# Kernel tuning notes

Hardware: AMD Instinct MI355X
Metric: run time of the kernel (lower is better)

## Reference

```python
import jax, jax.numpy as jnp
import numpy as np

N, E = 50000, 800000
IN_F, OUT_F = 256, 128


def setup_inputs() -> dict:
    key = jax.random.key(0)
    ks = jax.random.split(key, 12)
    s = 1.0 / np.sqrt(OUT_F)
    si = 1.0 / np.sqrt(IN_F)
    return {
        "h": jax.random.normal(ks[0], (N, IN_F), jnp.float32),
        "degrees": jax.random.randint(ks[1], (E, 6), 0, 5).astype(jnp.float32),
        "norm": jax.random.uniform(ks[2], (N, 1), jnp.float32, 0.05, 1.0),
        "src": jax.random.randint(ks[3], (E,), 0, N, jnp.int32),
        "dst": jax.random.randint(ks[4], (E,), 0, N, jnp.int32),
        "W_self": jax.random.normal(ks[5], (IN_F, OUT_F), jnp.float32) * si,
        "b_self": jax.random.normal(ks[6], (OUT_F,), jnp.float32) * si,
        "W_node": jax.random.normal(ks[7], (IN_F, 6 * OUT_F), jnp.float32) * si,
        "b_node": jax.random.normal(ks[8], (6 * OUT_F,), jnp.float32) * si,
        "W_edge": jax.random.normal(ks[9], (6, OUT_F), jnp.float32) * 0.4,
        "bias": jax.random.normal(ks[10], (1, OUT_F), jnp.float32) * 2 * s - s,
    }


def reference(h, degrees, norm, src, dst, W_self, b_self, W_node, b_node, W_edge, bias):
    n = h.shape[0]
    out = W_self.shape[1]
    # node-level linears
    h_node_msg = (h @ W_node + b_node).reshape(n, 6, out)  # [N,6,out]
    h_node_self = h @ W_self + b_self                       # [N,out]
    # edge-level linear (no bias)
    msg = degrees @ W_edge                                  # [E,out]
    mask = (degrees > 0).astype(h.dtype)                    # [E,6]
    # masked sum over the 6 degree-conditioned slices (gather per slice to
    # avoid materializing an [E,6,out] tensor)
    for i in range(6):
        msg = msg + h_node_msg[src, i] * mask[:, i:i + 1]
    msg = msg * norm[src]                                   # src-side norm
    accum = jax.ops.segment_sum(msg, dst, num_segments=n) * norm  # dst-side norm
    return jax.nn.relu(accum + h_node_self + bias)
```

## Files before the change

kernel.cpp:

```cpp
#include <hip/hip_runtime.h>
#include <stdint.h>

#define IN_F 256
#define OUT_F 128
#define NCOLS 1024
#define PROW 1280
#define BM 64
#define BN 128
#define BK 32

using bf16x8 = __attribute__((ext_vector_type(8))) __bf16;
using f32x4  = __attribute__((ext_vector_type(4))) float;
using f32x2  = __attribute__((ext_vector_type(2))) float;

static __device__ __forceinline__ unsigned short f2bf(float f) {
    unsigned u = __float_as_uint(f);
    u = u + 0x7fffu + ((u >> 16) & 1u);
    return (unsigned short)(u >> 16);
}
static __device__ __forceinline__ float bf_lo(unsigned u) { return __uint_as_float(u << 16); }
static __device__ __forceinline__ float bf_hi(unsigned u) { return __uint_as_float(u & 0xffff0000u); }

static __device__ __forceinline__ void async_load16(const void* g, void* l) {
    __builtin_amdgcn_global_load_lds(
        (__attribute__((address_space(1))) void*)g,
        (__attribute__((address_space(3))) void*)l,
        16, 0, 0);
}

__global__ void k_conv_h(const float* __restrict__ h, unsigned short* __restrict__ hb, int total8) {
    int i = blockIdx.x * blockDim.x + threadIdx.x;
    if (i >= total8) return;
    const float4* src = ((const float4*)h) + (size_t)i * 2;
    float4 a = src[0], b = src[1];
    union { unsigned short us[8]; uint4 v; } u;
    u.us[0] = f2bf(a.x); u.us[1] = f2bf(a.y); u.us[2] = f2bf(a.z); u.us[3] = f2bf(a.w);
    u.us[4] = f2bf(b.x); u.us[5] = f2bf(b.y); u.us[6] = f2bf(b.z); u.us[7] = f2bf(b.w);
    ((uint4*)hb)[i] = u.v;
}

__global__ void k_conv_w(const float* __restrict__ Wn, const float* __restrict__ Ws,
                         const float* __restrict__ bn, const float* __restrict__ bs,
                         unsigned short* __restrict__ Wt, float* __restrict__ bvec, int total) {
    int i = blockIdx.x * blockDim.x + threadIdx.x;
    if (i >= total) return;
    int k = i >> 10, c = i & 1023;
    float v;
    if (c < 768) {
        v = Wn[(size_t)k * 768 + c];
    } else if (c < 896) {
        int j = c - 768; v = 0.f;
#pragma unroll
        for (int s = 0; s < 6; ++s) v += Wn[(size_t)k * 768 + s * 128 + j];
    } else {
        v = Ws[(size_t)k * 128 + (c - 896)];
    }
    Wt[(size_t)c * IN_F + k] = f2bf(v);

    if (i < NCOLS) {
        float b;
        if (i < 768) b = bn[i];
        else if (i < 896) {
            int j = i - 768; b = 0.f;
#pragma unroll
            for (int s = 0; s < 6; ++s) b += bn[s * 128 + j];
        } else b = bs[i - 896];
        bvec[i] = b;
    }
}

__global__ void __launch_bounds__(256) k_gemm(
    const unsigned short* __restrict__ hb,
    const unsigned short* __restrict__ Wt,
    const float* __restrict__ bvec,
    const float* __restrict__ norm,
    char* __restrict__ PG, int N, int rowsPerXcd)
{
    __shared__ char lds[(BM + BN) * BK * 2];
    char* Ab = lds;
    char* Bb = lds + BM * BK * 2;

    const int f  = blockIdx.x;
    const int xc = f & 7;
    const int j  = f >> 3;
    const int rs = xc * rowsPerXcd + (j >> 3);
    const int ct = j & 7;
    const int r0 = rs * BM;
    if (r0 >= N) return;
    const int c0 = ct * BN;

    const int tid = threadIdx.x;
    const int wid = tid >> 6, lane = tid & 63;
    const int lrow = lane & 15, s = lane >> 4;
    const int wr = wid >> 1, wc = wid & 1;

    const int arow = tid >> 2;
    const int achunk = (tid & 3) ^ ((arow >> 1) & 3);
    int agrow = r0 + arow; if (agrow >= N) agrow = N - 1;
    const unsigned short* aseg = hb + (size_t)agrow * IN_F + achunk * 8;

    const int bcol0 = tid >> 2;
    const int bchunk0 = (tid & 3) ^ ((bcol0 >> 1) & 3);
    const unsigned short* bseg0 = Wt + (size_t)(c0 + bcol0) * IN_F + bchunk0 * 8;
    const int idx1 = tid + 256;
    const int bcol1 = idx1 >> 2;
    const int bchunk1 = (idx1 & 3) ^ ((bcol1 >> 1) & 3);
    const unsigned short* bseg1 = Wt + (size_t)(c0 + bcol1) * IN_F + bchunk1 * 8;

    int a_off[2], b_off[4];
#pragma unroll
    for (int m = 0; m < 2; ++m) {
        int rl = wr * 32 + m * 16 + lrow;
        a_off[m] = rl * 64 + ((s ^ ((rl >> 1) & 3)) << 4);
    }
#pragma unroll
    for (int n = 0; n < 4; ++n) {
        int cl = wc * 64 + n * 16 + lrow;
        b_off[n] = cl * 64 + ((s ^ ((cl >> 1) & 3)) << 4);
    }

    float nrmv[2][4];
#pragma unroll
    for (int m = 0; m < 2; ++m)
#pragma unroll
        for (int r = 0; r < 4; ++r) {
            int rg = r0 + wr * 32 + m * 16 + s * 4 + r;
            nrmv[m][r] = norm[rg < N ? rg : N - 1];
        }

    f32x4 acc[2][4] = {};

    for (int kk = 0; kk < IN_F / BK; ++kk) {
        async_load16(aseg + kk * BK, Ab + tid * 16);
        async_load16(bseg0 + kk * BK, Bb + tid * 16);
        async_load16(bseg1 + kk * BK, Bb + (tid + 256) * 16);
        __syncthreads();

        bf16x8 af[2], bfv[4];
#pragma unroll
        for (int m = 0; m < 2; ++m) af[m] = *(const bf16x8*)(Ab + a_off[m]);
#pragma unroll
        for (int n = 0; n < 4; ++n) bfv[n] = *(const bf16x8*)(Bb + b_off[n]);
#pragma unroll
        for (int m = 0; m < 2; ++m)
#pragma unroll
            for (int n = 0; n < 4; ++n)
                acc[m][n] = __builtin_amdgcn_mfma_f32_16x16x32_bf16(af[m], bfv[n], acc[m][n], 0, 0, 0);
        __syncthreads();
    }

    float bvn[4];
#pragma unroll
    for (int n = 0; n < 4; ++n) bvn[n] = bvec[c0 + wc * 64 + n * 16 + lrow];

    if (ct < 6) {
#pragma unroll
        for (int m = 0; m < 2; ++m) {
#pragma unroll
            for (int r = 0; r < 4; ++r) {
                const int rg = r0 + wr * 32 + m * 16 + s * 4 + r;
                const float sc = nrmv[m][r];
                float v0 = (acc[m][0][r] + bvn[0]) * sc;
                float v1 = (acc[m][1][r] + bvn[1]) * sc;
                float v2 = (acc[m][2][r] + bvn[2]) * sc;
                float v3 = (acc[m][3][r] + bvn[3]) * sc;
                int d = __builtin_amdgcn_cvt_pk_fp8_f32(v0, v1, 0, false);
                d = __builtin_amdgcn_cvt_pk_fp8_f32(v2, v3, d, true);
                if (rg < N)
                    *(int*)(PG + (size_t)rg * PROW + ct * 128 + (wc * 16 + lrow) * 4) = d;
            }
        }
    } else {
        const bool doN = (ct == 6);
        const int boff = doN ? 768 : 1024;
#pragma unroll
        for (int m = 0; m < 2; ++m) {
#pragma unroll
            for (int r = 0; r < 4; ++r) {
                const int rg = r0 + wr * 32 + m * 16 + s * 4 + r;
                const float sc = doN ? nrmv[m][r] : 1.f;
                float v0 = (acc[m][0][r] + bvn[0]) * sc;
                float v1 = (acc[m][1][r] + bvn[1]) * sc;
                float v2 = (acc[m][2][r] + bvn[2]) * sc;
                float v3 = (acc[m][3][r] + bvn[3]) * sc;
                uint2 dd;
                dd.x = (unsigned)f2bf(v0) | ((unsigned)f2bf(v1) << 16);
                dd.y = (unsigned)f2bf(v2) | ((unsigned)f2bf(v3) << 16);
                if (rg < N)
                    *(uint2*)(PG + (size_t)rg * PROW + boff + (wc * 32 + 2 * lrow) * 4) = dd;
            }
        }
    }
}

__global__ void k_hist(const int* __restrict__ dst, int* __restrict__ counts, int E) {
    int e = blockIdx.x * blockDim.x + threadIdx.x;
    if (e < E) atomicAdd(&counts[dst[e]], 1);
}

__global__ void __launch_bounds__(256) k_scan_a(const int* __restrict__ counts,
                                                int* __restrict__ offs,
                                                int* __restrict__ bsum, int N) {
    __shared__ int sm[256];
    int tid = threadIdx.x;
    int i = blockIdx.x * 256 + tid;
    int v = (i < N) ? counts[i] : 0;
    sm[tid] = v;
    __syncthreads();
#pragma unroll
    for (int st = 1; st < 256; st <<= 1) {
        int t = (tid >= st) ? sm[tid - st] : 0;
        __syncthreads();
        sm[tid] += t;
        __syncthreads();
    }
    if (i < N) offs[i] = sm[tid] - v;
    if (tid == 255) bsum[blockIdx.x] = sm[255];
}

__global__ void __launch_bounds__(256) k_scan_b(int* __restrict__ bsum, int NB) {
    __shared__ int sm[256];
    int tid = threadIdx.x;
    int v = (tid < NB) ? bsum[tid] : 0;
    sm[tid] = v;
    __syncthreads();
#pragma unroll
    for (int st = 1; st < 256; st <<= 1) {
        int t = (tid >= st) ? sm[tid - st] : 0;
        __syncthreads();
        sm[tid] += t;
        __syncthreads();
    }
    if (tid < NB) bsum[tid] = sm[tid] - v;
}

__global__ void k_scan_c(int* __restrict__ offs, const int* __restrict__ bsum,
                         int* __restrict__ cursor, int N) {
    int i = blockIdx.x * 256 + threadIdx.x;
    if (i >= N) return;
    int o = offs[i] + bsum[blockIdx.x];
    offs[i] = o;
    cursor[i] = o;
}

__global__ void k_scatter(const int* __restrict__ src, const int* __restrict__ dst,
                          const float* __restrict__ degrees,
                          int* __restrict__ cursor, uint2* __restrict__ pedge, int E) {
    int e = blockIdx.x * blockDim.x + threadIdx.x;
    if (e >= E) return;
    int d = dst[e];
    int slot = atomicAdd(&cursor[d], 1);
    unsigned pk = 0;
#pragma unroll
    for (int i = 0; i < 6; ++i) {
        float df = degrees[(size_t)e * 6 + i];
        pk |= ((unsigned)df) << (4 * i);
    }
    pedge[slot] = make_uint2((unsigned)src[e], pk);
}

__global__ void __launch_bounds__(256) k_aggregate(
    const char* __restrict__ PG,
    const int* __restrict__ row_start, const int* __restrict__ counts,
    const uint2* __restrict__ pedge,
    const float* __restrict__ norm, const float* __restrict__ W_edge,
    const float* __restrict__ bias, float* __restrict__ out, int N)
{
    __shared__ unsigned ELS[4][64];
    __shared__ unsigned ELF[4][192];
    const int wid = threadIdx.x >> 6;
    const int n = blockIdx.x * 4 + wid;
    if (n >= N) return;
    const int lane = threadIdx.x & 63;
    unsigned* els = ELS[wid];
    unsigned* elf = ELF[wid];

    const int cA = (lane >> 5) * 64 + (lane & 1) * 32 + ((lane >> 1) & 15);
    const int cB = cA + 16;

    float wA[6], wB[6];
#pragma unroll
    for (int i = 0; i < 6; ++i) {
        wA[i] = W_edge[i * OUT_F + cA];
        wB[i] = W_edge[i * OUT_F + cB];
    }

    const int beg = row_start[n];
    const int end = beg + counts[n];

    float Swd[6] = {0.f, 0.f, 0.f, 0.f, 0.f, 0.f};
    float g0 = 0.f, g1 = 0.f;

    for (int p0 = beg; p0 < end; p0 += 64) {
        const int t = p0 + lane;
        uint2 pe = (t < end) ? pedge[t] : make_uint2(0u, 0u);
        const unsigned dp = pe.y;
        const float nr = (dp != 0u) ? norm[pe.x] : 0.f;

        unsigned zm = 0;
#pragma unroll
        for (int i = 0; i < 6; ++i) {
            int d = (dp >> (4 * i)) & 15;
            if (d == 0) zm |= (1u << i);
            Swd[i] += nr * (float)d;
        }
        const int z = __popc(zm);
        int ns, nf;
        if (dp == 0u)      { ns = 0; nf = 0; }
        else if (z <= 2)   { ns = 1; nf = z; }
        else               { ns = 0; nf = 6 - z; }

        int x = (ns << 16) | nf;
#pragma unroll
        for (int st = 1; st < 64; st <<= 1) {
            int v = __shfl_up(x, st);
            if (lane >= st) x += v;
        }
        const int tot = __shfl(x, 63);
        x -= (ns << 16) | nf;
        const int exS = x >> 16, exF = x & 0xffff;
        const int totS = tot >> 16, totF = tot & 0xffff;

        if (dp != 0u) {
            const unsigned base = pe.x * (unsigned)PROW;
            if (z <= 2) {
                els[exS] = base + 768u;
                int wp = exF;
#pragma unroll
                for (int i = 0; i < 6; ++i)
                    if ((zm >> i) & 1u) elf[wp++] = (base + i * 128u) | 0x80000000u;
            } else {
                int wp = exF;
#pragma unroll
                for (int i = 0; i < 6; ++i)
                    if (!((zm >> i) & 1u)) elf[wp++] = base + i * 128u;
            }
        }
        asm volatile("s_waitcnt lgkmcnt(0)" ::: "memory");

        int j = 0;
        for (; j + 4 <= totS; j += 4) {
            unsigned a0 = els[j], a1 = els[j + 1], a2 = els[j + 2], a3 = els[j + 3];
            unsigned u0 = *(const unsigned*)(PG + a0 + lane * 4);
            unsigned u1 = *(const unsigned*)(PG + a1 + lane * 4);
            unsigned u2 = *(const unsigned*)(PG + a2 + lane * 4);
            unsigned u3 = *(const unsigned*)(PG + a3 + lane * 4);
            g0 += bf_lo(u0); g1 += bf_hi(u0);
            g0 += bf_lo(u1); g1 += bf_hi(u1);
            g0 += bf_lo(u2); g1 += bf_hi(u2);
            g0 += bf_lo(u3); g1 += bf_hi(u3);
        }
        for (; j < totS; ++j) {
            unsigned u0 = *(const unsigned*)(PG + els[j] + lane * 4);
            g0 += bf_lo(u0); g1 += bf_hi(u0);
        }

        j = 0;
        for (; j + 4 <= totF; j += 4) {
            unsigned e0 = elf[j], e1 = elf[j + 1], e2 = elf[j + 2], e3 = elf[j + 3];
            unsigned short q0 = *(const unsigned short*)(PG + (e0 & 0x7fffffffu) + lane * 2);
            unsigned short q1 = *(const unsigned short*)(PG + (e1 & 0x7fffffffu) + lane * 2);
            unsigned short q2 = *(const unsigned short*)(PG + (e2 & 0x7fffffffu) + lane * 2);
            unsigned short q3 = *(const unsigned short*)(PG + (e3 & 0x7fffffffu) + lane * 2);
            f32x2 f0 = __builtin_amdgcn_cvt_pk_f32_fp8((int)q0, false);
            f32x2 f1 = __builtin_amdgcn_cvt_pk_f32_fp8((int)q1, false);
            f32x2 f2 = __builtin_amdgcn_cvt_pk_f32_fp8((int)q2, false);
            f32x2 f3 = __builtin_amdgcn_cvt_pk_f32_fp8((int)q3, false);
            float s0 = __uint_as_float(0x3f800000u | (e0 & 0x80000000u));
            float s1 = __uint_as_float(0x3f800000u | (e1 & 0x80000000u));
            float s2 = __uint_as_float(0x3f800000u | (e2 & 0x80000000u));
            float s3 = __uint_as_float(0x3f800000u | (e3 & 0x80000000u));
            g0 += s0 * f0.x; g1 += s0 * f0.y;
            g0 += s1 * f1.x; g1 += s1 * f1.y;
            g0 += s2 * f2.x; g1 += s2 * f2.y;
            g0 += s3 * f3.x; g1 += s3 * f3.y;
        }
        for (; j < totF; ++j) {
            unsigned e0 = elf[j];
            unsigned short q0 = *(const unsigned short*)(PG + (e0 & 0x7fffffffu) + lane * 2);
            f32x2 f0 = __builtin_amdgcn_cvt_pk_f32_fp8((int)q0, false);
            float s0 = __uint_as_float(0x3f800000u | (e0 & 0x80000000u));
            g0 += s0 * f0.x; g1 += s0 * f0.y;
        }
    }

    float b0 = 0.f, b1 = 0.f;
#pragma unroll
    for (int i = 0; i < 6; ++i) {
        float v = Swd[i];
#pragma unroll
        for (int st = 1; st < 64; st <<= 1) v += __shfl_xor(v, st);
        b0 += v * wA[i];
        b1 += v * wB[i];
    }

    const unsigned us = *(const unsigned*)(PG + (size_t)n * PROW + 1024 + lane * 4);
    const float nd = norm[n];
    float o0 = fmaxf((g0 + b0) * nd + bf_lo(us) + bias[cA], 0.f);
    float o1 = fmaxf((g1 + b1) * nd + bf_hi(us) + bias[cB], 0.f);
    out[(size_t)n * OUT_F + cA] = o0;
    out[(size_t)n * OUT_F + cB] = o1;
}

extern "C" void kernel_launch(void* const* d_in, const int* in_sizes, int n_in,
                              void* d_out, int out_size, void* d_ws, size_t ws_size,
                              hipStream_t stream)
{
    const float* h       = (const float*)d_in[0];
    const float* degrees = (const float*)d_in[1];
    const float* norm    = (const float*)d_in[2];
    const int*   src     = (const int*)d_in[3];
    const int*   dst     = (const int*)d_in[4];
    const float* W_self  = (const float*)d_in[5];
    const float* b_self  = (const float*)d_in[6];
    const float* W_node  = (const float*)d_in[7];
    const float* b_node  = (const float*)d_in[8];
    const float* W_edge  = (const float*)d_in[9];
    const float* bias    = (const float*)d_in[10];
    float* out = (float*)d_out;

    const int N = in_sizes[2];
    const int E = in_sizes[3];
    const int NB = (N + 255) / 256;

    char* ws = (char*)d_ws;
    size_t off = 0;
    auto alloc = [&](size_t sz) { size_t o = off; off = (off + sz + 255) & ~(size_t)255; return o; };
    char*           PG     = (char*)(ws + alloc((size_t)N * PROW));
    unsigned short* hb     = (unsigned short*)(ws + alloc((size_t)N * IN_F * 2));
    unsigned short* Wt     = (unsigned short*)(ws + alloc((size_t)NCOLS * IN_F * 2));
    float*          bvec   = (float*)(ws + alloc(NCOLS * 4));
    int*            counts = (int*)(ws + alloc((size_t)N * 4));
    int*            offs   = (int*)(ws + alloc((size_t)N * 4));
    int*            cursor = (int*)(ws + alloc((size_t)N * 4));
    int*            bsum   = (int*)(ws + alloc((size_t)NB * 4));
    uint2*          pedge  = (uint2*)(ws + alloc((size_t)E * 8));

    hipMemsetAsync(counts, 0, (size_t)N * 4, stream);

    int t8 = N * (IN_F / 8);
    k_conv_h<<<(t8 + 255) / 256, 256, 0, stream>>>(h, hb, t8);

    int tw = IN_F * NCOLS;
    k_conv_w<<<(tw + 255) / 256, 256, 0, stream>>>(W_node, W_self, b_node, b_self, Wt, bvec, tw);

    const int R  = (N + BM - 1) / BM;
    const int RP = (R + 7) / 8;
    k_gemm<<<RP * 8 * 8, 256, 0, stream>>>(hb, Wt, bvec, norm, PG, N, RP);

    k_hist<<<(E + 255) / 256, 256, 0, stream>>>(dst, counts, E);
    k_scan_a<<<NB, 256, 0, stream>>>(counts, offs, bsum, N);
    k_scan_b<<<1, 256, 0, stream>>>(bsum, NB);
    k_scan_c<<<NB, 256, 0, stream>>>(offs, bsum, cursor, N);
    k_scatter<<<(E + 255) / 256, 256, 0, stream>>>(src, dst, degrees, cursor, pedge, E);

    k_aggregate<<<(N + 3) / 4, 256, 0, stream>>>(PG, offs, counts, pedge, norm, W_edge, bias, out, N);
}
```

Baseline: 248.8 us.

## Interleave per-node message slices into 1KB rows, drop summed-slice GEMM columns

The projected-feature buffer is re-laid out so each node row is 1024 bytes, with each lane's six fp8 slice values plus its bf16 self term packed contiguously in 16 bytes. The GEMM no longer computes the extra 'sum of all six slices' column tile, so the grid drops from eight to seven column tiles. The aggregation kernel replaces its per-wavefront prefix-scan compaction of nonzero slices with one 16-byte load per edge and mask-multiplied FMAs. This trades the sparse-gather bookkeeping for always loading all six slices per edge, and it uses scattered 2-byte stores in the GEMM epilogue.

```diff
diff --git a/kernel.cpp b/kernel.cpp
--- a/kernel.cpp
+++ b/kernel.cpp
@@ -3,8 +3,8 @@
 
 #define IN_F 256
 #define OUT_F 128
-#define NCOLS 1024
-#define PROW 1280
+#define NCOLSG 896
+#define PROW 1024
 #define BM 64
 #define BN 128
 #define BK 32
@@ -44,29 +44,10 @@
                          unsigned short* __restrict__ Wt, float* __restrict__ bvec, int total) {
     int i = blockIdx.x * blockDim.x + threadIdx.x;
     if (i >= total) return;
-    int k = i >> 10, c = i & 1023;
-    float v;
-    if (c < 768) {
-        v = Wn[(size_t)k * 768 + c];
-    } else if (c < 896) {
-        int j = c - 768; v = 0.f;
-#pragma unroll
-        for (int s = 0; s < 6; ++s) v += Wn[(size_t)k * 768 + s * 128 + j];
-    } else {
-        v = Ws[(size_t)k * 128 + (c - 896)];
-    }
+    int k = i / NCOLSG, c = i - k * NCOLSG;
+    float v = (c < 768) ? Wn[(size_t)k * 768 + c] : Ws[(size_t)k * 128 + (c - 768)];
     Wt[(size_t)c * IN_F + k] = f2bf(v);
-
-    if (i < NCOLS) {
-        float b;
-        if (i < 768) b = bn[i];
-        else if (i < 896) {
-            int j = i - 768; b = 0.f;
-#pragma unroll
-            for (int s = 0; s < 6; ++s) b += bn[s * 128 + j];
-        } else b = bs[i - 896];
-        bvec[i] = b;
-    }
+    if (i < NCOLSG) bvec[i] = (i < 768) ? bn[i] : bs[i - 768];
 }
 
 __global__ void __launch_bounds__(256) k_gemm(
@@ -83,8 +64,8 @@
     const int f  = blockIdx.x;
     const int xc = f & 7;
     const int j  = f >> 3;
-    const int rs = xc * rowsPerXcd + (j >> 3);
-    const int ct = j & 7;
+    const int rs = xc * rowsPerXcd + j / 7;
+    const int ct = j % 7;
     const int r0 = rs * BM;
     if (r0 >= N) return;
     const int c0 = ct * BN;
@@ -152,6 +133,7 @@
     float bvn[4];
 #pragma unroll
     for (int n = 0; n < 4; ++n) bvn[n] = bvec[c0 + wc * 64 + n * 16 + lrow];
+    const int L0 = wc * 32 + 2 * lrow;
 
     if (ct < 6) {
 #pragma unroll
@@ -159,35 +141,33 @@
 #pragma unroll
             for (int r = 0; r < 4; ++r) {
                 const int rg = r0 + wr * 32 + m * 16 + s * 4 + r;
+                if (rg >= N) continue;
                 const float sc = nrmv[m][r];
                 float v0 = (acc[m][0][r] + bvn[0]) * sc;
                 float v1 = (acc[m][1][r] + bvn[1]) * sc;
                 float v2 = (acc[m][2][r] + bvn[2]) * sc;
                 float v3 = (acc[m][3][r] + bvn[3]) * sc;
-                int d = __builtin_amdgcn_cvt_pk_fp8_f32(v0, v1, 0, false);
-                d = __builtin_amdgcn_cvt_pk_fp8_f32(v2, v3, d, true);
-                if (rg < N)
-                    *(int*)(PG + (size_t)rg * PROW + ct * 128 + (wc * 16 + lrow) * 4) = d;
+                int p01 = __builtin_amdgcn_cvt_pk_fp8_f32(v0, v1, 0, false);
+                int p23 = __builtin_amdgcn_cvt_pk_fp8_f32(v2, v3, 0, false);
+                char* base = PG + ((size_t)rg << 10) + L0 * 16 + ct * 2;
+                *(unsigned short*)(base)      = (unsigned short)p01;
+                *(unsigned short*)(base + 16) = (unsigned short)p23;
             }
         }
     } else {
-        const bool doN = (ct == 6);
-        const int boff = doN ? 768 : 1024;
 #pragma unroll
         for (int m = 0; m < 2; ++m) {
 #pragma unroll
             for (int r = 0; r < 4; ++r) {
                 const int rg = r0 + wr * 32 + m * 16 + s * 4 + r;
-                const float sc = doN ? nrmv[m][r] : 1.f;
-                float v0 = (acc[m][0][r] + bvn[0]) * sc;
-                float v1 = (acc[m][1][r] + bvn[1]) * sc;
-                float v2 = (acc[m][2][r] + bvn[2]) * sc;
-                float v3 = (acc[m][3][r] + bvn[3]) * sc;
-                uint2 dd;
-                dd.x = (unsigned)f2bf(v0) | ((unsigned)f2bf(v1) << 16);
-                dd.y = (unsigned)f2bf(v2) | ((unsigned)f2bf(v3) << 16);
-                if (rg < N)
-                    *(uint2*)(PG + (size_t)rg * PROW + boff + (wc * 32 + 2 * lrow) * 4) = dd;
+                if (rg >= N) continue;
+                float v0 = acc[m][0][r] + bvn[0];
+                float v1 = acc[m][1][r] + bvn[1];
+                float v2 = acc[m][2][r] + bvn[2];
+                float v3 = acc[m][3][r] + bvn[3];
+                char* base = PG + ((size_t)rg << 10) + L0 * 16 + 12;
+                *(unsigned*)(base)      = (unsigned)f2bf(v0) | ((unsigned)f2bf(v1) << 16);
+                *(unsigned*)(base + 16) = (unsigned)f2bf(v2) | ((unsigned)f2bf(v3) << 16);
             }
         }
     }
@@ -259,6 +239,22 @@
     pedge[slot] = make_uint2((unsigned)src[e], pk);
 }
 
+static __device__ __forceinline__ void edge_proc(uint4 v, unsigned dp, float& g0, float& g1) {
+    f32x2 f; float m;
+    m = (dp & 0x00000Fu) ? 1.f : 0.f; f = __builtin_amdgcn_cvt_pk_f32_fp8((int)v.x, false);
+    g0 = fmaf(m, f.x, g0); g1 = fmaf(m, f.y, g1);
+    m = (dp & 0x0000F0u) ? 1.f : 0.f; f = __builtin_amdgcn_cvt_pk_f32_fp8((int)v.x, true);
+    g0 = fmaf(m, f.x, g0); g1 = fmaf(m, f.y, g1);
+    m = (dp & 0x000F00u) ? 1.f : 0.f; f = __builtin_amdgcn_cvt_pk_f32_fp8((int)v.y, false);
+    g0 = fmaf(m, f.x, g0); g1 = fmaf(m, f.y, g1);
+    m = (dp & 0x00F000u) ? 1.f : 0.f; f = __builtin_amdgcn_cvt_pk_f32_fp8((int)v.y, true);
+    g0 = fmaf(m, f.x, g0); g1 = fmaf(m, f.y, g1);
+    m = (dp & 0x0F0000u) ? 1.f : 0.f; f = __builtin_amdgcn_cvt_pk_f32_fp8((int)v.z, false);
+    g0 = fmaf(m, f.x, g0); g1 = fmaf(m, f.y, g1);
+    m = (dp & 0xF00000u) ? 1.f : 0.f; f = __builtin_amdgcn_cvt_pk_f32_fp8((int)v.z, true);
+    g0 = fmaf(m, f.x, g0); g1 = fmaf(m, f.y, g1);
+}
+
 __global__ void __launch_bounds__(256) k_aggregate(
     const char* __restrict__ PG,
     const int* __restrict__ row_start, const int* __restrict__ counts,
@@ -266,17 +262,15 @@
     const float* __restrict__ norm, const float* __restrict__ W_edge,
     const float* __restrict__ bias, float* __restrict__ out, int N)
 {
-    __shared__ unsigned ELS[4][64];
-    __shared__ unsigned ELF[4][192];
+    __shared__ uint2 EB[4][64];
     const int wid = threadIdx.x >> 6;
     const int n = blockIdx.x * 4 + wid;
     if (n >= N) return;
     const int lane = threadIdx.x & 63;
-    unsigned* els = ELS[wid];
-    unsigned* elf = ELF[wid];
 
     const int cA = (lane >> 5) * 64 + (lane & 1) * 32 + ((lane >> 1) & 15);
     const int cB = cA + 16;
+    const int laneB = lane * 16;
 
     float wA[6], wB[6];
 #pragma unroll
@@ -296,91 +290,36 @@
         uint2 pe = (t < end) ? pedge[t] : make_uint2(0u, 0u);
         const unsigned dp = pe.y;
         const float nr = (dp != 0u) ? norm[pe.x] : 0.f;
-
-        unsigned zm = 0;
 #pragma unroll
         for (int i = 0; i < 6; ++i) {
             int d = (dp >> (4 * i)) & 15;
-            if (d == 0) zm |= (1u << i);
             Swd[i] += nr * (float)d;
         }
-        const int z = __popc(zm);
-        int ns, nf;
-        if (dp == 0u)      { ns = 0; nf = 0; }
-        else if (z <= 2)   { ns = 1; nf = z; }
-        else               { ns = 0; nf = 6 - z; }
-
-        int x = (ns << 16) | nf;
-#pragma unroll
-        for (int st = 1; st < 64; st <<= 1) {
-            int v = __shfl_up(x, st);
-            if (lane >= st) x += v;
-        }
-        const int tot = __shfl(x, 63);
-        x -= (ns << 16) | nf;
-        const int exS = x >> 16, exF = x & 0xffff;
-        const int totS = tot >> 16, totF = tot & 0xffff;
-
-        if (dp != 0u) {
-            const unsigned base = pe.x * (unsigned)PROW;
-            if (z <= 2) {
-                els[exS] = base + 768u;
-                int wp = exF;
-#pragma unroll
-                for (int i = 0; i < 6; ++i)
-                    if ((zm >> i) & 1u) elf[wp++] = (base + i * 128u) | 0x80000000u;
-            } else {
-                int wp = exF;
-#pragma unroll
-                for (int i = 0; i < 6; ++i)
-                    if (!((zm >> i) & 1u)) elf[wp++] = base + i * 128u;
-            }
-        }
+        EB[wid][lane] = pe;
         asm volatile("s_waitcnt lgkmcnt(0)" ::: "memory");
 
-        int j = 0;
-        for (; j + 4 <= totS; j += 4) {
-            unsigned a0 = els[j], a1 = els[j + 1], a2 = els[j + 2], a3 = els[j + 3];
-            unsigned u0 = *(const unsigned*)(PG + a0 + lane * 4);
-            unsigned u1 = *(const unsigned*)(PG + a1 + lane * 4);
-            unsigned u2 = *(const unsigned*)(PG + a2 + lane * 4);
-            unsigned u3 = *(const unsigned*)(PG + a3 + lane * 4);
-            g0 += bf_lo(u0); g1 += bf_hi(u0);
-            g0 += bf_lo(u1); g1 += bf_hi(u1);
-            g0 += bf_lo(u2); g1 += bf_hi(u2);
-            g0 += bf_lo(u3); g1 += bf_hi(u3);
-        }
-        for (; j < totS; ++j) {
-            unsigned u0 = *(const unsigned*)(PG + els[j] + lane * 4);
-            g0 += bf_lo(u0); g1 += bf_hi(u0);
-        }
-
-        j = 0;
-        for (; j + 4 <= totF; j += 4) {
-            unsigned e0 = elf[j], e1 = elf[j + 1], e2 = elf[j + 2], e3 = elf[j + 3];
-            unsigned short q0 = *(const unsigned short*)(PG + (e0 & 0x7fffffffu) + lane * 2);
-            unsigned short q1 = *(const unsigned short*)(PG + (e1 & 0x7fffffffu) + lane * 2);
-            unsigned short q2 = *(const unsigned short*)(PG + (e2 & 0x7fffffffu) + lane * 2);
-            unsigned short q3 = *(const unsigned short*)(PG + (e3 & 0x7fffffffu) + lane * 2);
-            f32x2 f0 = __builtin_amdgcn_cvt_pk_f32_fp8((int)q0, false);
-            f32x2 f1 = __builtin_amdgcn_cvt_pk_f32_fp8((int)q1, false);
-            f32x2 f2 = __builtin_amdgcn_cvt_pk_f32_fp8((int)q2, false);
-            f32x2 f3 = __builtin_amdgcn_cvt_pk_f32_fp8((int)q3, false);
-            float s0 = __uint_as_float(0x3f800000u | (e0 & 0x80000000u));
-            float s1 = __uint_as_float(0x3f800000u | (e1 & 0x80000000u));
-            float s2 = __uint_as_float(0x3f800000u | (e2 & 0x80000000u));
-            float s3 = __uint_as_float(0x3f800000u | (e3 & 0x80000000u));
-            g0 += s0 * f0.x; g1 += s0 * f0.y;
-            g0 += s1 * f1.x; g1 += s1 * f1.y;
-            g0 += s2 * f2.x; g1 += s2 * f2.y;
-            g0 += s3 * f3.x; g1 += s3 * f3.y;
-        }
-        for (; j < totF; ++j) {
-            unsigned e0 = elf[j];
-            unsigned short q0 = *(const unsigned short*)(PG + (e0 & 0x7fffffffu) + lane * 2);
-            f32x2 f0 = __builtin_amdgcn_cvt_pk_f32_fp8((int)q0, false);
-            float s0 = __uint_as_float(0x3f800000u | (e0 & 0x80000000u));
-            g0 += s0 * f0.x; g1 += s0 * f0.y;
+        const int cnt = min(64, end - p0);
+        int tt = 0;
+        for (; tt + 4 <= cnt; tt += 4) {
+            uint2 e0 = EB[wid][tt], e1 = EB[wid][tt + 1], e2 = EB[wid][tt + 2], e3 = EB[wid][tt + 3];
+            const char* r0p = PG + ((size_t)__builtin_amdgcn_readfirstlane(e0.x) << 10);
+            const char* r1p = PG + ((size_t)__builtin_amdgcn_readfirstlane(e1.x) << 10);
+            const char* r2p = PG + ((size_t)__builtin_amdgcn_readfirstlane(e2.x) << 10);
+            const char* r3p = PG + ((size_t)__builtin_amdgcn_readfirstlane(e3.x) << 10);
+            uint4 v0 = *(const uint4*)(r0p + laneB);
+            uint4 v1 = *(const uint4*)(r1p + laneB);
+            uint4 v2 = *(const uint4*)(r2p + laneB);
+            uint4 v3 = *(const uint4*)(r3p + laneB);
+            edge_proc(v0, __builtin_amdgcn_readfirstlane(e0.y), g0, g1);
+            edge_proc(v1, __builtin_amdgcn_readfirstlane(e1.y), g0, g1);
+            edge_proc(v2, __builtin_amdgcn_readfirstlane(e2.y), g0, g1);
+            edge_proc(v3, __builtin_amdgcn_readfirstlane(e3.y), g0, g1);
+        }
+        for (; tt < cnt; ++tt) {
+            uint2 e0 = EB[wid][tt];
+            const char* r0p = PG + ((size_t)__builtin_amdgcn_readfirstlane(e0.x) << 10);
+            uint4 v0 = *(const uint4*)(r0p + laneB);
+            edge_proc(v0, __builtin_amdgcn_readfirstlane(e0.y), g0, g1);
         }
     }
 
@@ -394,7 +333,7 @@
         b1 += v * wB[i];
     }
 
-    const unsigned us = *(const unsigned*)(PG + (size_t)n * PROW + 1024 + lane * 4);
+    const unsigned us = *(const unsigned*)(PG + ((size_t)n << 10) + laneB + 12);
     const float nd = norm[n];
     float o0 = fmaxf((g0 + b0) * nd + bf_lo(us) + bias[cA], 0.f);
     float o1 = fmaxf((g1 + b1) * nd + bf_hi(us) + bias[cB], 0.f);
@@ -428,8 +367,8 @@
     auto alloc = [&](size_t sz) { size_t o = off; off = (off + sz + 255) & ~(size_t)255; return o; };
     char*           PG     = (char*)(ws + alloc((size_t)N * PROW));
     unsigned short* hb     = (unsigned short*)(ws + alloc((size_t)N * IN_F * 2));
-    unsigned short* Wt     = (unsigned short*)(ws + alloc((size_t)NCOLS * IN_F * 2));
-    float*          bvec   = (float*)(ws + alloc(NCOLS * 4));
+    unsigned short* Wt     = (unsigned short*)(ws + alloc((size_t)NCOLSG * IN_F * 2));
+    float*          bvec   = (float*)(ws + alloc(NCOLSG * 4));
     int*            counts = (int*)(ws + alloc((size_t)N * 4));
     int*            offs   = (int*)(ws + alloc((size_t)N * 4));
     int*            cursor = (int*)(ws + alloc((size_t)N * 4));
@@ -441,12 +380,12 @@
     int t8 = N * (IN_F / 8);
     k_conv_h<<<(t8 + 255) / 256, 256, 0, stream>>>(h, hb, t8);
 
-    int tw = IN_F * NCOLS;
+    int tw = IN_F * NCOLSG;
     k_conv_w<<<(tw + 255) / 256, 256, 0, stream>>>(W_node, W_self, b_node, b_self, Wt, bvec, tw);
 
     const int R  = (N + BM - 1) / BM;
     const int RP = (R + 7) / 8;
-    k_gemm<<<RP * 8 * 8, 256, 0, stream>>>(hb, Wt, bvec, norm, PG, N, RP);
+    k_gemm<<<RP * 8 * 7, 256, 0, stream>>>(hb, Wt, bvec, norm, PG, N, RP);
 
     k_hist<<<(E + 255) / 256, 256, 0, stream>>>(dst, counts, E);
     k_scan_a<<<NB, 256, 0, stream>>>(counts, offs, bsum, N);
```

After: 313.6 us. 26.1% more time.
